# Kernel tuning notes

Measured on AMD Instinct MI355X. Metric: run time of the kernel, lower is better.

## Reference

```python
import jax, jax.numpy as jnp
import numpy as np

NEG_SLOPE = 0.2


def gat_layer(x, adj, W, a_src, a_dst):
    # x: (C, in_dim), adj: (C, C) 0/1, W: (in_dim, H*D), a_src/a_dst: (H, D)
    C = x.shape[0]
    H, D = a_src.shape
    h = (x @ W).reshape(C, H, D)            # (C, H, D)
    hh = jnp.transpose(h, (1, 0, 2))        # (H, C, D)
    asrc = jnp.einsum('hcd,hd->hc', hh, a_src)  # (H, C)
    adst = jnp.einsum('hcd,hd->hc', hh, a_dst)  # (H, C)
    e = asrc[:, :, None] + adst[:, None, :]     # (H, C, C)
    e = jax.nn.leaky_relu(e, NEG_SLOPE)
    e = jnp.where(adj[None, :, :] == 0, -jnp.inf, e)
    attn = jax.nn.softmax(e, axis=-1)           # (H, C, C)
    out = jnp.einsum('hij,hjd->hid', attn, hh)  # (H, C, D)
    return jnp.transpose(out, (1, 0, 2)).reshape(C, H * D)


def setup_inputs() -> dict:
    key = jax.random.key(0)
    ks = jax.random.split(key, 12)
    B, doc_dim = 1024, 768
    C, label_dim = 4096, 768
    hidden, H = 512, 4
    D = hidden // H  # 128

    doc_x = jax.random.normal(ks[0], (B, doc_dim), dtype=jnp.float32)
    label_init = jax.random.normal(ks[1], (C, label_dim), dtype=jnp.float32)
    adj = jax.random.randint(ks[2], (C, C), 0, 2, dtype=jnp.int32)
    adj = adj.at[jnp.arange(C), jnp.arange(C)].set(1)  # self-loops

    def xavier(k, shape):
        fan_in, fan_out = shape[0], shape[1]
        lim = jnp.sqrt(6.0 / (fan_in + fan_out)).astype(jnp.float32)
        return jax.random.uniform(k, shape, jnp.float32, -lim, lim)

    W1 = xavier(ks[3], (label_dim, hidden))
    a_src1 = xavier(ks[4], (H, D))
    a_dst1 = xavier(ks[5], (H, D))
    W2 = xavier(ks[6], (hidden, hidden))
    a_src2 = xavier(ks[7], (H, D))
    a_dst2 = xavier(ks[8], (H, D))
    Wd = xavier(ks[9], (doc_dim, hidden))
    bd = jnp.zeros((hidden,), jnp.float32)
    return {"doc_x": doc_x, "label_init": label_init, "adj": adj,
            "W1": W1, "a_src1": a_src1, "a_dst1": a_dst1,
            "W2": W2, "a_src2": a_src2, "a_dst2": a_dst2,
            "Wd": Wd, "bd": bd}


def reference(doc_x, label_init, adj, W1, a_src1, a_dst1, W2, a_src2, a_dst2, Wd, bd):
    # doc_proj (dropout = identity in eval)
    doc_h = jax.nn.relu(doc_x @ Wd + bd)            # (B, hidden)
    # label encoder: GAT -> ELU -> GAT
    h = gat_layer(label_init, adj, W1, a_src1, a_dst1)
    h = jax.nn.elu(h)
    label_h = gat_layer(h, adj, W2, a_src2, a_dst2)  # (C, hidden)
    logits = doc_h @ label_h.T                      # (B, C)
    return logits
```

## Files before the change

### kernel.cpp

```cpp
#include <hip/hip_runtime.h>
#include <hip/hip_bf16.h>
#include <math.h>

#define BDOCS   1024
#define CNODES  4096
#define INDIM   768
#define HID     512
#define NHEAD   4
#define HDIM    128
#define NEG_SLOPE 0.2f

typedef __attribute__((ext_vector_type(8))) short short8;
typedef __attribute__((ext_vector_type(4))) float f32x4;

__device__ __forceinline__ float lrelu(float x) { return x > 0.f ? x : NEG_SLOPE * x; }

__device__ __forceinline__ short f2bf(float f) {
    union { float f; unsigned u; } v; v.f = f;
    unsigned r = (v.u + 0x7fff + ((v.u >> 16) & 1)) >> 16;
    return (short)r;
}
__device__ __forceinline__ unsigned pk2(float a, float b) {
    union { float f; unsigned u; } x, y; x.f = a; y.f = b;
    unsigned lo = (x.u + 0x7fff + ((x.u >> 16) & 1)) >> 16;
    unsigned hi = (y.u + 0x7fff + ((y.u >> 16) & 1)) >> 16;
    return lo | (hi << 16);
}
__device__ __forceinline__ short hup(float f) {
    union { float f; unsigned u; } v; v.f = f;
    return (short)((v.u + 0x8000) >> 16);
}

__global__ __launch_bounds__(256)
void pack_adj(const int* __restrict__ adj, unsigned long long* __restrict__ adjb64)
{
    const int t    = threadIdx.x;
    const int gw   = blockIdx.x * 4 + (t >> 6);
    const int lane = t & 63;
    const int i  = gw >> 6;
    const int j0 = (gw & 63) * 64;
    const int a  = adj[(size_t)i * CNODES + j0 + lane];
    const unsigned long long m = __ballot(a != 0);
    if (lane == 0) adjb64[(size_t)i * 64 + (j0 >> 6)] = m;
}

__global__ __launch_bounds__(256)
void frag_T(const float* __restrict__ src, short* __restrict__ dst, int N, int K)
{
    __shared__ float tile[32][132];
    const int jc = blockIdx.x;
    const int nq = blockIdx.y;
    const int t  = threadIdx.x;
    const int KC = K >> 5;
#pragma unroll
    for (int it = 0; it < 16; it++) {
        const int e = it * 256 + t;
        const int j = e >> 7, n = e & 127;
        tile[j][n] = src[(size_t)(jc * 32 + j) * N + nq * 128 + n];
    }
    __syncthreads();
#pragma unroll
    for (int s = 0; s < 2; s++) {
        const int item = s * 256 + t;
        const int nbl = item >> 6, lane = item & 63;
        const int nr = lane & 15, kq = lane >> 4;
        short8 v;
#pragma unroll
        for (int jr = 0; jr < 8; jr++)
            v[jr] = f2bf(tile[kq * 8 + jr][nbl * 16 + nr]);
        *(short8*)&dst[((size_t)((nq * 8 + nbl) * KC + jc) * 64 + lane) * 8] = v;
    }
}

__global__ __launch_bounds__(256)
void frag_A(const float* __restrict__ src, short* __restrict__ dst, int C)
{
    __shared__ float tile[16][132];
    const int rb = blockIdx.x, cq = blockIdx.y;
    const int t  = threadIdx.x;
    const int KC = C >> 5;
#pragma unroll
    for (int it = 0; it < 8; it++) {
        const int e = it * 256 + t;
        const int r = e >> 7, c = e & 127;
        tile[r][c] = src[(size_t)(rb * 16 + r) * C + cq * 128 + c];
    }
    __syncthreads();
    const int kcl = t >> 6, lane = t & 63;
    const int m = lane & 15, kq = lane >> 4;
    short8 v8;
#pragma unroll
    for (int j = 0; j < 8; j++) v8[j] = f2bf(tile[m][kcl * 32 + kq * 8 + j]);
    *(short8*)&dst[((size_t)(rb * KC + cq * 4 + kcl) * 64 + lane) * 8] = v8;
}

template <int KC>
__global__ __launch_bounds__(64)
void gemm_hpre(const short* __restrict__ Af, const short* __restrict__ Bf,
               const float* __restrict__ a_src, const float* __restrict__ a_dst,
               short* __restrict__ hbTf, float* __restrict__ asrc, float* __restrict__ adst)
{
    __shared__ __align__(16) short tileT[128][56];
    const int lane = threadIdx.x;
    const int mb0  = blockIdx.x * 2;
    const int nq   = blockIdx.y;
    const int i0   = blockIdx.x * 32;

    f32x4 acc[2][8];
#pragma unroll
    for (int f = 0; f < 2; f++)
#pragma unroll
        for (int c = 0; c < 8; c++) acc[f][c] = (f32x4){0.f, 0.f, 0.f, 0.f};

    const short* ap0 = Af + (size_t)mb0 * KC * 512 + lane * 8;
    const short* ap1 = ap0 + (size_t)KC * 512;
    const short* bp  = Bf + (size_t)(nq * 8) * KC * 512 + lane * 8;

#pragma unroll 2
    for (int kc = 0; kc < KC; kc++) {
        short8 a0 = *(const short8*)(ap0 + (size_t)kc * 512);
        short8 a1 = *(const short8*)(ap1 + (size_t)kc * 512);
        short8 bf[8];
#pragma unroll
        for (int c = 0; c < 8; c++)
            bf[c] = *(const short8*)(bp + ((size_t)c * KC + kc) * 512);
#pragma unroll
        for (int c = 0; c < 8; c++) {
            acc[0][c] = __builtin_amdgcn_mfma_f32_16x16x32_bf16(a0, bf[c], acc[0][c], 0, 0, 0);
            acc[1][c] = __builtin_amdgcn_mfma_f32_16x16x32_bf16(a1, bf[c], acc[1][c], 0, 0, 0);
        }
    }

    const int col = lane & 15, q4 = lane >> 4;

#pragma unroll
    for (int f = 0; f < 2; f++)
#pragma unroll
        for (int c = 0; c < 8; c++) {
            unsigned d0 = pk2(acc[f][c][0], acc[f][c][1]);
            unsigned d1 = pk2(acc[f][c][2], acc[f][c][3]);
            uint2 u; u.x = d0; u.y = d1;
            *(uint2*)&tileT[c * 16 + col][f * 16 + q4 * 4] = u;
        }
    __syncthreads();
    {
        const int nr = lane & 15, kq = lane >> 4;
#pragma unroll
        for (int nbl = 0; nbl < 8; nbl++) {
            short8 v = *(const short8*)&tileT[nbl * 16 + nr][kq * 8];
            *(short8*)&hbTf[(((size_t)(nq * 8 + nbl) * (CNODES / 32) + blockIdx.x) * 64 + lane) * 8] = v;
        }
    }

    float ssrc[2][4] = {}, sdst[2][4] = {};
#pragma unroll
    for (int c = 0; c < 8; c++) {
        const float vs = a_src[nq * 128 + c * 16 + col];
        const float vd = a_dst[nq * 128 + c * 16 + col];
#pragma unroll
        for (int f = 0; f < 2; f++)
#pragma unroll
            for (int r = 0; r < 4; r++) {
                ssrc[f][r] += acc[f][c][r] * vs;
                sdst[f][r] += acc[f][c][r] * vd;
            }
    }
#pragma unroll
    for (int mask = 1; mask <= 8; mask <<= 1)
#pragma unroll
        for (int f = 0; f < 2; f++)
#pragma unroll
            for (int r = 0; r < 4; r++) {
                ssrc[f][r] += __shfl_xor(ssrc[f][r], mask);
                sdst[f][r] += __shfl_xor(sdst[f][r], mask);
            }
    if (col == 0) {
#pragma unroll
        for (int f = 0; f < 2; f++)
#pragma unroll
            for (int r = 0; r < 4; r++) {
                const int row = i0 + f * 16 + q4 * 4 + r;
                asrc[nq * CNODES + row] = ssrc[f][r];
                adst[nq * CNODES + row] = sdst[f][r];
            }
    }
}

template <int KC>
__global__ __launch_bounds__(64)
void gemm_doc(const short* __restrict__ Af, const short* __restrict__ Bf,
              const float* __restrict__ bias, short* __restrict__ dhf)
{
    __shared__ __align__(16) short tile[16][128];
    const int lane = threadIdx.x;
    const int mb = blockIdx.x;
    const int nq = blockIdx.y;

    f32x4 acc[8];
#pragma unroll
    for (int c = 0; c < 8; c++) acc[c] = (f32x4){0.f, 0.f, 0.f, 0.f};

    const short* ap = Af + (size_t)mb * KC * 512 + lane * 8;
    const short* bp = Bf + (size_t)(nq * 8) * KC * 512 + lane * 8;

#pragma unroll 2
    for (int kc = 0; kc < KC; kc++) {
        short8 a = *(const short8*)(ap + (size_t)kc * 512);
#pragma unroll
        for (int c = 0; c < 8; c++) {
            short8 bf = *(const short8*)(bp + ((size_t)c * KC + kc) * 512);
            acc[c] = __builtin_amdgcn_mfma_f32_16x16x32_bf16(a, bf, acc[c], 0, 0, 0);
        }
    }

    const int col = lane & 15, q4 = lane >> 4;
#pragma unroll
    for (int c = 0; c < 8; c++)
#pragma unroll
        for (int r = 0; r < 4; r++) {
            float v = fmaxf(acc[c][r] + bias[nq * 128 + c * 16 + col], 0.f);
            tile[q4 * 4 + r][c * 16 + col] = f2bf(v);
        }
    __syncthreads();
    const int m = lane & 15, kq = lane >> 4;
#pragma unroll
    for (int kcl = 0; kcl < 4; kcl++) {
        short8 v = *(const short8*)&tile[m][kcl * 32 + kq * 8];
        *(short8*)&dhf[(((size_t)mb * 16 + nq * 4 + kcl) * 64 + lane) * 8] = v;
    }
}

template <int KC>
__global__ __launch_bounds__(64)
void gemm_frag(const short* __restrict__ Af, const short* __restrict__ Bf,
               float* __restrict__ Cmat, int N)
{
    const int lane = threadIdx.x;
    const int mb0  = blockIdx.x * 2;
    const int nq   = blockIdx.y;

    f32x4 acc[2][8];
#pragma unroll
    for (int f = 0; f < 2; f++)
#pragma unroll
        for (int c = 0; c < 8; c++) acc[f][c] = (f32x4){0.f, 0.f, 0.f, 0.f};

    const short* ap0 = Af + (size_t)mb0 * KC * 512 + lane * 8;
    const short* ap1 = ap0 + (size_t)KC * 512;
    const short* bp  = Bf + (size_t)(nq * 8) * KC * 512 + lane * 8;

#pragma unroll 2
    for (int kc = 0; kc < KC; kc++) {
        short8 a0 = *(const short8*)(ap0 + (size_t)kc * 512);
        short8 a1 = *(const short8*)(ap1 + (size_t)kc * 512);
        short8 bf[8];
#pragma unroll
        for (int c = 0; c < 8; c++)
            bf[c] = *(const short8*)(bp + ((size_t)c * KC + kc) * 512);
#pragma unroll
        for (int c = 0; c < 8; c++) {
            acc[0][c] = __builtin_amdgcn_mfma_f32_16x16x32_bf16(a0, bf[c], acc[0][c], 0, 0, 0);
            acc[1][c] = __builtin_amdgcn_mfma_f32_16x16x32_bf16(a1, bf[c], acc[1][c], 0, 0, 0);
        }
    }

    const int col = lane & 15, q4 = lane >> 4;
#pragma unroll
    for (int f = 0; f < 2; f++)
#pragma unroll
        for (int c = 0; c < 8; c++)
#pragma unroll
            for (int r = 0; r < 4; r++) {
                const int row = (mb0 + f) * 16 + q4 * 4 + r;
                Cmat[(size_t)row * N + nq * 128 + c * 16 + col] = acc[f][c][r];
            }
}

__global__ __launch_bounds__(256)
void adst_max(const float* __restrict__ adst, float* __restrict__ Mh)
{
    const int h = blockIdx.x, t = threadIdx.x;
    __shared__ float red[256];
    float m = -1e30f;
    for (int j = t; j < CNODES; j += 256) m = fmaxf(m, adst[h * CNODES + j]);
    red[t] = m; __syncthreads();
    for (int s = 128; s >= 1; s >>= 1) {
        if (t < s) red[t] = fmaxf(red[t], red[t + s]);
        __syncthreads();
    }
    if (t == 0) Mh[h] = red[0];
}

__global__ __launch_bounds__(256)
void exp_dst(const float* __restrict__ adst, const float* __restrict__ Mh,
             float* __restrict__ E1, float* __restrict__ E2)
{
    const int idx = blockIdx.x * 256 + threadIdx.x;
    const int h = idx >> 12;
    const float d = adst[idx] - Mh[h];
    E1[idx] = __expf(d);
    E2[idx] = __expf(0.2f * d);
}

__global__ __launch_bounds__(256, 2)
void attn_pv(const short* __restrict__ hbTf,
             const unsigned int* __restrict__ adjb,
             const float* __restrict__ asrc,
             const float* __restrict__ E1, const float* __restrict__ E2,
             const float* __restrict__ Mh,
             float* __restrict__ part, float* __restrict__ lpart,
             int jper)
{
    const int t    = threadIdx.x;
    const int w    = t >> 6;
    const int lane = t & 63;
    const int m    = lane & 15;
    const int kq   = lane >> 4;
    const int i0   = blockIdx.x * 32;
    const int ks   = blockIdx.y;
    const int js   = ks * jper;

    const float mh  = Mh[w];
    const float as0 = asrc[w * CNODES + i0 + m];
    const float as1 = asrc[w * CNODES + i0 + 16 + m];
    const float mr0 = lrelu(as0 + mh), mr1 = lrelu(as1 + mh);
    const float A10 = __expf(as0 + mh - mr0),        A11 = __expf(as1 + mh - mr1);
    const float A20 = __expf(0.2f * (as0 + mh) - mr0), A21 = __expf(0.2f * (as1 + mh) - mr1);
    const float T00 = __expf(-as0 - mh),             T01 = __expf(-as1 - mh);

    f32x4 acc[2][8], accO[2];
#pragma unroll
    for (int f = 0; f < 2; f++) {
        accO[f] = (f32x4){0.f, 0.f, 0.f, 0.f};
#pragma unroll
        for (int c = 0; c < 8; c++) acc[f][c] = (f32x4){0.f, 0.f, 0.f, 0.f};
    }
    short8 ones;
#pragma unroll
    for (int q = 0; q < 8; q++) ones[q] = (short)0x3F80;

    const unsigned int* ar0 = adjb + (size_t)(i0 + m) * 128 + (js >> 5);
    const unsigned int* ar1 = adjb + (size_t)(i0 + 16 + m) * 128 + (js >> 5);
    const int nchunks = jper >> 5;

    for (int ch = 0; ch < nchunks; ch++) {
        const int j0 = js + ch * 32;
        const unsigned int aw0 = ar0[ch] >> (kq * 8);
        const unsigned int aw1 = ar1[ch] >> (kq * 8);
        const float4* p1 = (const float4*)(E1 + (size_t)w * CNODES + j0 + kq * 8);
        const float4* p2 = (const float4*)(E2 + (size_t)w * CNODES + j0 + kq * 8);
        const float4 x0 = p1[0], x1 = p1[1];
        const float4 y0 = p2[0], y1 = p2[1];
        const float e1v[8] = {x0.x, x0.y, x0.z, x0.w, x1.x, x1.y, x1.z, x1.w};
        const float e2v[8] = {y0.x, y0.y, y0.z, y0.w, y1.x, y1.y, y1.z, y1.w};

        short8 bf[8];
        const short* bbase = hbTf + (((size_t)(w * 8) * 128 + (j0 >> 5)) * 64 + lane) * 8;
#pragma unroll
        for (int c = 0; c < 8; c++)
            bf[c] = *(const short8*)(bbase + (size_t)c * 128 * 64 * 8);

        short8 a0, a1;
#pragma unroll
        for (int q = 0; q < 8; q++) {
            const float e1 = e1v[q], e2 = e2v[q];
            const bool c0 = e1 > T00, c1 = e1 > T01;
            float w0 = (c0 ? A10 : A20) * (c0 ? e1 : e2);
            float w1 = (c1 ? A11 : A21) * (c1 ? e1 : e2);
            w0 = ((aw0 >> q) & 1u) ? w0 : 0.f;
            w1 = ((aw1 >> q) & 1u) ? w1 : 0.f;
            a0[q] = hup(w0);
            a1[q] = hup(w1);
        }

#pragma unroll
        for (int c = 0; c < 8; c++) {
            acc[0][c] = __builtin_amdgcn_mfma_f32_16x16x32_bf16(a0, bf[c], acc[0][c], 0, 0, 0);
            acc[1][c] = __builtin_amdgcn_mfma_f32_16x16x32_bf16(a1, bf[c], acc[1][c], 0, 0, 0);
        }
        accO[0] = __builtin_amdgcn_mfma_f32_16x16x32_bf16(a0, ones, accO[0], 0, 0, 0);
        accO[1] = __builtin_amdgcn_mfma_f32_16x16x32_bf16(a1, ones, accO[1], 0, 0, 0);
    }

    const int col = lane & 15, q4 = lane >> 4;
    if (col == 0) {
#pragma unroll
        for (int f = 0; f < 2; f++)
#pragma unroll
            for (int r = 0; r < 4; r++)
                lpart[((size_t)ks * NHEAD + w) * CNODES + i0 + f * 16 + q4 * 4 + r] = accO[f][r];
    }

    float* pbase = part + (size_t)ks * CNODES * HID;
#pragma unroll
    for (int f = 0; f < 2; f++)
#pragma unroll
        for (int c = 0; c < 8; c++)
#pragma unroll
            for (int r = 0; r < 4; r++) {
                const int row = i0 + f * 16 + q4 * 4 + r;
                pbase[(size_t)row * HID + w * HDIM + c * 16 + col] = acc[f][c][r];
            }
}

template <bool ELU>
__global__ __launch_bounds__(256)
void reduce_norm_frag(const float* __restrict__ part, const float* __restrict__ lpart,
                      short* __restrict__ dst, int KS)
{
    const int t = threadIdx.x;
    const int W = blockIdx.x * 4 + (t >> 6);
    const int lane = t & 63;
    const int rb = W >> 4, kc = W & 15;
    const int m = lane & 15, kq = lane >> 4;
    const int i = rb * 16 + m;
    const int n0 = kc * 32 + kq * 8;
    const int h = kc >> 2;

    float v[8] = {};
    float l = 0.f;
    for (int s = 0; s < KS; s++) {
        const float* p = part + (size_t)s * CNODES * HID + (size_t)i * HID + n0;
        const float4 a = ((const float4*)p)[0], b = ((const float4*)p)[1];
        v[0] += a.x; v[1] += a.y; v[2] += a.z; v[3] += a.w;
        v[4] += b.x; v[5] += b.y; v[6] += b.z; v[7] += b.w;
        l += lpart[((size_t)s * NHEAD + h) * CNODES + i];
    }
    const float inv = 1.0f / l;
    short8 o;
#pragma unroll
    for (int q = 0; q < 8; q++) {
        float x = v[q] * inv;
        if (ELU) x = x > 0.f ? x : (__expf(x) - 1.f);
        o[q] = f2bf(x);
    }
    *(short8*)&dst[((size_t)(rb * 16 + kc) * 64 + lane) * 8] = o;
}

extern "C" void kernel_launch(void* const* d_in, const int* in_sizes, int n_in,
                              void* d_out, int out_size, void* d_ws, size_t ws_size,
                              hipStream_t stream)
{
    const float* doc_x      = (const float*)d_in[0];
    const float* label_init = (const float*)d_in[1];
    const int*   adj        = (const int*)d_in[2];
    const float* W1         = (const float*)d_in[3];
    const float* a_src1     = (const float*)d_in[4];
    const float* a_dst1     = (const float*)d_in[5];
    const float* W2         = (const float*)d_in[6];
    const float* a_src2     = (const float*)d_in[7];
    const float* a_dst2     = (const float*)d_in[8];
    const float* Wd         = (const float*)d_in[9];
    const float* bd         = (const float*)d_in[10];
    float*       out        = (float*)d_out;

    char* wsb = (char*)d_ws;
    size_t off = 0;
    auto alloc = [&](size_t bytes) -> char* {
        char* p = wsb + off;
        off = (off + bytes + 255) & ~(size_t)255;
        return p;
    };

    float* asrc  = (float*)alloc(NHEAD * CNODES * 4);
    float* adst  = (float*)alloc(NHEAD * CNODES * 4);
    float* Mh    = (float*)alloc(256);
    float* E1    = (float*)alloc(NHEAD * CNODES * 4);
    float* E2    = (float*)alloc(NHEAD * CNODES * 4);
    float* lpart = (float*)alloc((size_t)8 * NHEAD * CNODES * 4);
    unsigned int* adjb = (unsigned int*)alloc((size_t)CNODES * 128 * 4);
    short* hbTf  = (short*)alloc((size_t)CNODES * HID * 2);
    short* Wdf   = (short*)alloc((size_t)INDIM * HID * 2);
    short* W1f   = (short*)alloc((size_t)INDIM * HID * 2);
    short* W2f   = (short*)alloc((size_t)HID * HID * 2);
    short* dxf   = (short*)alloc((size_t)BDOCS * INDIM * 2);
    short* Af_li = (short*)alloc((size_t)CNODES * INDIM * 2);
    short* Af2   = (short*)alloc((size_t)CNODES * HID * 2);
    short* lhf   = (short*)alloc((size_t)CNODES * HID * 2);
    short* dhf   = (short*)alloc((size_t)BDOCS * HID * 2);
    float* part  = (float*)(wsb + off);

    int KS = 4;
    const size_t slice_bytes = (size_t)CNODES * HID * 4;
    while (KS > 1 && off + (size_t)KS * slice_bytes > ws_size) KS >>= 1;
    const int jper = CNODES / KS;

    const dim3 blk(256);

    pack_adj<<<CNODES * CNODES / 64 / 4, blk, 0, stream>>>(adj, (unsigned long long*)adjb);
    frag_T<<<dim3(INDIM / 32, HID / 128), blk, 0, stream>>>(Wd, Wdf, HID, INDIM);
    frag_T<<<dim3(INDIM / 32, HID / 128), blk, 0, stream>>>(W1, W1f, HID, INDIM);
    frag_T<<<dim3(HID / 32, HID / 128), blk, 0, stream>>>(W2, W2f, HID, HID);
    frag_A<<<dim3(BDOCS / 16, INDIM / 128), blk, 0, stream>>>(doc_x, dxf, INDIM);
    frag_A<<<dim3(CNODES / 16, INDIM / 128), blk, 0, stream>>>(label_init, Af_li, INDIM);

    gemm_doc<INDIM / 32><<<dim3(BDOCS / 16, HID / 128), 64, 0, stream>>>(dxf, Wdf, bd, dhf);

    gemm_hpre<INDIM / 32><<<dim3(CNODES / 32, NHEAD), 64, 0, stream>>>(
        Af_li, W1f, a_src1, a_dst1, hbTf, asrc, adst);

    adst_max<<<NHEAD, 256, 0, stream>>>(adst, Mh);
    exp_dst<<<NHEAD * CNODES / 256, blk, 0, stream>>>(adst, Mh, E1, E2);
    attn_pv<<<dim3(CNODES / 32, KS), blk, 0, stream>>>(hbTf, adjb, asrc, E1, E2, Mh, part, lpart, jper);
    reduce_norm_frag<true><<<CNODES * HID / 256 / 8, blk, 0, stream>>>(part, lpart, Af2, KS);

    gemm_hpre<HID / 32><<<dim3(CNODES / 32, NHEAD), 64, 0, stream>>>(
        Af2, W2f, a_src2, a_dst2, hbTf, asrc, adst);

    adst_max<<<NHEAD, 256, 0, stream>>>(adst, Mh);
    exp_dst<<<NHEAD * CNODES / 256, blk, 0, stream>>>(adst, Mh, E1, E2);
    attn_pv<<<dim3(CNODES / 32, KS), blk, 0, stream>>>(hbTf, adjb, asrc, E1, E2, Mh, part, lpart, jper);
    reduce_norm_frag<false><<<CNODES * HID / 256 / 8, blk, 0, stream>>>(part, lpart, lhf, KS);

    gemm_frag<HID / 32><<<dim3(BDOCS / 32, CNODES / 128), 64, 0, stream>>>(dhf, lhf, out, CNODES);
}
```

Before: 411.6 us.

## Shrink GEMM tiles, fuse softmax stats, bf16 split-K partials with KSPLIT=8

Halves the per-block tile in gemm_hpre (16 rows) and gemm_doc (64 columns) so more blocks fill the GPU. Merges adst_max and exp_dst into one 1024-thread kernel. Fixes the attention split-K at 8 and stores the partials in bf16 through an LDS-staged coalesced write, which halves the traffic of the partials and of the reduce pass. attn_pv also gets occupancy hint 3 and loop unroll 2. Storing partials in bf16 costs accuracy, and the workspace is no longer checked against ws_size.

```diff
diff --git a/kernel.cpp b/kernel.cpp
--- a/kernel.cpp
+++ b/kernel.cpp
@@ -10,6 +10,10 @@
 #define HDIM    128
 #define NEG_SLOPE 0.2f
 
+#define KSPLIT  8
+#define JPER    (CNODES / KSPLIT)
+#define NCH     (JPER / 32)
+
 typedef __attribute__((ext_vector_type(8))) short short8;
 typedef __attribute__((ext_vector_type(4))) float f32x4;
 
@@ -19,6 +23,10 @@
     union { float f; unsigned u; } v; v.f = f;
     unsigned r = (v.u + 0x7fff + ((v.u >> 16) & 1)) >> 16;
     return (short)r;
+}
+__device__ __forceinline__ float bf2f(short s) {
+    union { float f; unsigned u; } v; v.u = ((unsigned)(unsigned short)s) << 16;
+    return v.f;
 }
 __device__ __forceinline__ unsigned pk2(float a, float b) {
     union { float f; unsigned u; } x, y; x.f = a; y.f = b;
@@ -100,11 +108,131 @@
                const float* __restrict__ a_src, const float* __restrict__ a_dst,
                short* __restrict__ hbTf, float* __restrict__ asrc, float* __restrict__ adst)
 {
-    __shared__ __align__(16) short tileT[128][56];
+    __shared__ __align__(16) short tileT[128][24];
+    const int lane = threadIdx.x;
+    const int mb   = blockIdx.x;
+    const int nq   = blockIdx.y;
+    const int i0   = mb * 16;
+
+    f32x4 acc[8];
+#pragma unroll
+    for (int c = 0; c < 8; c++) acc[c] = (f32x4){0.f, 0.f, 0.f, 0.f};
+
+    const short* ap = Af + (size_t)mb * KC * 512 + lane * 8;
+    const short* bp = Bf + (size_t)(nq * 8) * KC * 512 + lane * 8;
+
+#pragma unroll 2
+    for (int kc = 0; kc < KC; kc++) {
+        short8 a = *(const short8*)(ap + (size_t)kc * 512);
+#pragma unroll
+        for (int c = 0; c < 8; c++) {
+            short8 bf = *(const short8*)(bp + ((size_t)c * KC + kc) * 512);
+            acc[c] = __builtin_amdgcn_mfma_f32_16x16x32_bf16(a, bf, acc[c], 0, 0, 0);
+        }
+    }
+
+    const int col = lane & 15, q4 = lane >> 4;
+
+#pragma unroll
+    for (int c = 0; c < 8; c++) {
+        uint2 u;
+        u.x = pk2(acc[c][0], acc[c][1]);
+        u.y = pk2(acc[c][2], acc[c][3]);
+        *(uint2*)&tileT[c * 16 + col][q4 * 4] = u;
+    }
+    __syncthreads();
+    {
+        const int jc = mb >> 1, khalf = mb & 1;
+        const int nr = lane & 15, kq = lane >> 4;
+        if ((kq >> 1) == khalf) {
+#pragma unroll
+            for (int nbl = 0; nbl < 8; nbl++) {
+                short8 v = *(const short8*)&tileT[nbl * 16 + nr][(kq & 1) * 8];
+                *(short8*)&hbTf[(((size_t)(nq * 8 + nbl) * (CNODES / 32) + jc) * 64 + lane) * 8] = v;
+            }
+        }
+    }
+
+    float ssrc[4] = {}, sdst[4] = {};
+#pragma unroll
+    for (int c = 0; c < 8; c++) {
+        const float vs = a_src[nq * 128 + c * 16 + col];
+        const float vd = a_dst[nq * 128 + c * 16 + col];
+#pragma unroll
+        for (int r = 0; r < 4; r++) {
+            ssrc[r] += acc[c][r] * vs;
+            sdst[r] += acc[c][r] * vd;
+        }
+    }
+#pragma unroll
+    for (int mask = 1; mask <= 8; mask <<= 1)
+#pragma unroll
+        for (int r = 0; r < 4; r++) {
+            ssrc[r] += __shfl_xor(ssrc[r], mask);
+            sdst[r] += __shfl_xor(sdst[r], mask);
+        }
+    if (col == 0) {
+#pragma unroll
+        for (int r = 0; r < 4; r++) {
+            const int row = i0 + q4 * 4 + r;
+            asrc[nq * CNODES + row] = ssrc[r];
+            adst[nq * CNODES + row] = sdst[r];
+        }
+    }
+}
+
+template <int KC>
+__global__ __launch_bounds__(64)
+void gemm_doc(const short* __restrict__ Af, const short* __restrict__ Bf,
+              const float* __restrict__ bias, short* __restrict__ dhf)
+{
+    __shared__ __align__(16) short tile[16][64];
+    const int lane = threadIdx.x;
+    const int mb = blockIdx.x;
+    const int ng = blockIdx.y;
+
+    f32x4 acc[4];
+#pragma unroll
+    for (int c = 0; c < 4; c++) acc[c] = (f32x4){0.f, 0.f, 0.f, 0.f};
+
+    const short* ap = Af + (size_t)mb * KC * 512 + lane * 8;
+    const short* bp = Bf + (size_t)(ng * 4) * KC * 512 + lane * 8;
+
+#pragma unroll 2
+    for (int kc = 0; kc < KC; kc++) {
+        short8 a = *(const short8*)(ap + (size_t)kc * 512);
+#pragma unroll
+        for (int c = 0; c < 4; c++) {
+            short8 bf = *(const short8*)(bp + ((size_t)c * KC + kc) * 512);
+            acc[c] = __builtin_amdgcn_mfma_f32_16x16x32_bf16(a, bf, acc[c], 0, 0, 0);
+        }
+    }
+
+    const int col = lane & 15, q4 = lane >> 4;
+#pragma unroll
+    for (int c = 0; c < 4; c++)
+#pragma unroll
+        for (int r = 0; r < 4; r++) {
+            float v = fmaxf(acc[c][r] + bias[ng * 64 + c * 16 + col], 0.f);
+            tile[q4 * 4 + r][c * 16 + col] = f2bf(v);
+        }
+    __syncthreads();
+    const int m = lane & 15, kq = lane >> 4;
+#pragma unroll
+    for (int kcl = 0; kcl < 2; kcl++) {
+        short8 v = *(const short8*)&tile[m][kcl * 32 + kq * 8];
+        *(short8*)&dhf[(((size_t)mb * 16 + ng * 2 + kcl) * 64 + lane) * 8] = v;
+    }
+}
+
+template <int KC>
+__global__ __launch_bounds__(64)
+void gemm_frag(const short* __restrict__ Af, const short* __restrict__ Bf,
+               float* __restrict__ Cmat, int N)
+{
     const int lane = threadIdx.x;
     const int mb0  = blockIdx.x * 2;
     const int nq   = blockIdx.y;
-    const int i0   = blockIdx.x * 32;
 
     f32x4 acc[2][8];
 #pragma unroll
@@ -132,139 +260,6 @@
     }
 
     const int col = lane & 15, q4 = lane >> 4;
-
-#pragma unroll
-    for (int f = 0; f < 2; f++)
-#pragma unroll
-        for (int c = 0; c < 8; c++) {
-            unsigned d0 = pk2(acc[f][c][0], acc[f][c][1]);
-            unsigned d1 = pk2(acc[f][c][2], acc[f][c][3]);
-            uint2 u; u.x = d0; u.y = d1;
-            *(uint2*)&tileT[c * 16 + col][f * 16 + q4 * 4] = u;
-        }
-    __syncthreads();
-    {
-        const int nr = lane & 15, kq = lane >> 4;
-#pragma unroll
-        for (int nbl = 0; nbl < 8; nbl++) {
-            short8 v = *(const short8*)&tileT[nbl * 16 + nr][kq * 8];
-            *(short8*)&hbTf[(((size_t)(nq * 8 + nbl) * (CNODES / 32) + blockIdx.x) * 64 + lane) * 8] = v;
-        }
-    }
-
-    float ssrc[2][4] = {}, sdst[2][4] = {};
-#pragma unroll
-    for (int c = 0; c < 8; c++) {
-        const float vs = a_src[nq * 128 + c * 16 + col];
-        const float vd = a_dst[nq * 128 + c * 16 + col];
-#pragma unroll
-        for (int f = 0; f < 2; f++)
-#pragma unroll
-            for (int r = 0; r < 4; r++) {
-                ssrc[f][r] += acc[f][c][r] * vs;
-                sdst[f][r] += acc[f][c][r] * vd;
-            }
-    }
-#pragma unroll
-    for (int mask = 1; mask <= 8; mask <<= 1)
-#pragma unroll
-        for (int f = 0; f < 2; f++)
-#pragma unroll
-            for (int r = 0; r < 4; r++) {
-                ssrc[f][r] += __shfl_xor(ssrc[f][r], mask);
-                sdst[f][r] += __shfl_xor(sdst[f][r], mask);
-            }
-    if (col == 0) {
-#pragma unroll
-        for (int f = 0; f < 2; f++)
-#pragma unroll
-            for (int r = 0; r < 4; r++) {
-                const int row = i0 + f * 16 + q4 * 4 + r;
-                asrc[nq * CNODES + row] = ssrc[f][r];
-                adst[nq * CNODES + row] = sdst[f][r];
-            }
-    }
-}
-
-template <int KC>
-__global__ __launch_bounds__(64)
-void gemm_doc(const short* __restrict__ Af, const short* __restrict__ Bf,
-              const float* __restrict__ bias, short* __restrict__ dhf)
-{
-    __shared__ __align__(16) short tile[16][128];
-    const int lane = threadIdx.x;
-    const int mb = blockIdx.x;
-    const int nq = blockIdx.y;
-
-    f32x4 acc[8];
-#pragma unroll
-    for (int c = 0; c < 8; c++) acc[c] = (f32x4){0.f, 0.f, 0.f, 0.f};
-
-    const short* ap = Af + (size_t)mb * KC * 512 + lane * 8;
-    const short* bp = Bf + (size_t)(nq * 8) * KC * 512 + lane * 8;
-
-#pragma unroll 2
-    for (int kc = 0; kc < KC; kc++) {
-        short8 a = *(const short8*)(ap + (size_t)kc * 512);
-#pragma unroll
-        for (int c = 0; c < 8; c++) {
-            short8 bf = *(const short8*)(bp + ((size_t)c * KC + kc) * 512);
-            acc[c] = __builtin_amdgcn_mfma_f32_16x16x32_bf16(a, bf, acc[c], 0, 0, 0);
-        }
-    }
-
-    const int col = lane & 15, q4 = lane >> 4;
-#pragma unroll
-    for (int c = 0; c < 8; c++)
-#pragma unroll
-        for (int r = 0; r < 4; r++) {
-            float v = fmaxf(acc[c][r] + bias[nq * 128 + c * 16 + col], 0.f);
-            tile[q4 * 4 + r][c * 16 + col] = f2bf(v);
-        }
-    __syncthreads();
-    const int m = lane & 15, kq = lane >> 4;
-#pragma unroll
-    for (int kcl = 0; kcl < 4; kcl++) {
-        short8 v = *(const short8*)&tile[m][kcl * 32 + kq * 8];
-        *(short8*)&dhf[(((size_t)mb * 16 + nq * 4 + kcl) * 64 + lane) * 8] = v;
-    }
-}
-
-template <int KC>
-__global__ __launch_bounds__(64)
-void gemm_frag(const short* __restrict__ Af, const short* __restrict__ Bf,
-               float* __restrict__ Cmat, int N)
-{
-    const int lane = threadIdx.x;
-    const int mb0  = blockIdx.x * 2;
-    const int nq   = blockIdx.y;
-
-    f32x4 acc[2][8];
-#pragma unroll
-    for (int f = 0; f < 2; f++)
-#pragma unroll
-        for (int c = 0; c < 8; c++) acc[f][c] = (f32x4){0.f, 0.f, 0.f, 0.f};
-
-    const short* ap0 = Af + (size_t)mb0 * KC * 512 + lane * 8;
-    const short* ap1 = ap0 + (size_t)KC * 512;
-    const short* bp  = Bf + (size_t)(nq * 8) * KC * 512 + lane * 8;
-
-#pragma unroll 2
-    for (int kc = 0; kc < KC; kc++) {
-        short8 a0 = *(const short8*)(ap0 + (size_t)kc * 512);
-        short8 a1 = *(const short8*)(ap1 + (size_t)kc * 512);
-        short8 bf[8];
-#pragma unroll
-        for (int c = 0; c < 8; c++)
-            bf[c] = *(const short8*)(bp + ((size_t)c * KC + kc) * 512);
-#pragma unroll
-        for (int c = 0; c < 8; c++) {
-            acc[0][c] = __builtin_amdgcn_mfma_f32_16x16x32_bf16(a0, bf[c], acc[0][c], 0, 0, 0);
-            acc[1][c] = __builtin_amdgcn_mfma_f32_16x16x32_bf16(a1, bf[c], acc[1][c], 0, 0, 0);
-        }
-    }
-
-    const int col = lane & 15, q4 = lane >> 4;
 #pragma unroll
     for (int f = 0; f < 2; f++)
 #pragma unroll
@@ -276,41 +271,41 @@
             }
 }
 
-__global__ __launch_bounds__(256)
-void adst_max(const float* __restrict__ adst, float* __restrict__ Mh)
-{
+__global__ __launch_bounds__(1024)
+void stats_exp(const float* __restrict__ adst, float* __restrict__ Mh,
+               float* __restrict__ E1, float* __restrict__ E2)
+{
+    __shared__ float red[1024];
+    __shared__ float s_mh;
     const int h = blockIdx.x, t = threadIdx.x;
-    __shared__ float red[256];
-    float m = -1e30f;
-    for (int j = t; j < CNODES; j += 256) m = fmaxf(m, adst[h * CNODES + j]);
+    const float4 d4 = *(const float4*)(adst + (size_t)h * CNODES + t * 4);
+    float m = fmaxf(fmaxf(d4.x, d4.y), fmaxf(d4.z, d4.w));
     red[t] = m; __syncthreads();
-    for (int s = 128; s >= 1; s >>= 1) {
+    for (int s = 512; s >= 1; s >>= 1) {
         if (t < s) red[t] = fmaxf(red[t], red[t + s]);
         __syncthreads();
     }
-    if (t == 0) Mh[h] = red[0];
-}
-
-__global__ __launch_bounds__(256)
-void exp_dst(const float* __restrict__ adst, const float* __restrict__ Mh,
-             float* __restrict__ E1, float* __restrict__ E2)
-{
-    const int idx = blockIdx.x * 256 + threadIdx.x;
-    const int h = idx >> 12;
-    const float d = adst[idx] - Mh[h];
-    E1[idx] = __expf(d);
-    E2[idx] = __expf(0.2f * d);
-}
-
-__global__ __launch_bounds__(256, 2)
+    if (t == 0) { s_mh = red[0]; Mh[h] = red[0]; }
+    __syncthreads();
+    const float mh = s_mh;
+    float4 e1, e2;
+    e1.x = __expf(d4.x - mh); e2.x = __expf(0.2f * (d4.x - mh));
+    e1.y = __expf(d4.y - mh); e2.y = __expf(0.2f * (d4.y - mh));
+    e1.z = __expf(d4.z - mh); e2.z = __expf(0.2f * (d4.z - mh));
+    e1.w = __expf(d4.w - mh); e2.w = __expf(0.2f * (d4.w - mh));
+    *(float4*)(E1 + (size_t)h * CNODES + t * 4) = e1;
+    *(float4*)(E2 + (size_t)h * CNODES + t * 4) = e2;
+}
+
+__global__ __launch_bounds__(256, 3)
 void attn_pv(const short* __restrict__ hbTf,
              const unsigned int* __restrict__ adjb,
              const float* __restrict__ asrc,
              const float* __restrict__ E1, const float* __restrict__ E2,
              const float* __restrict__ Mh,
-             float* __restrict__ part, float* __restrict__ lpart,
-             int jper)
-{
+             short* __restrict__ part, float* __restrict__ lpart)
+{
+    __shared__ __align__(16) short tileO[32][520];
     const int t    = threadIdx.x;
     const int w    = t >> 6;
     const int lane = t & 63;
@@ -318,15 +313,15 @@
     const int kq   = lane >> 4;
     const int i0   = blockIdx.x * 32;
     const int ks   = blockIdx.y;
-    const int js   = ks * jper;
+    const int js   = ks * JPER;
 
     const float mh  = Mh[w];
     const float as0 = asrc[w * CNODES + i0 + m];
     const float as1 = asrc[w * CNODES + i0 + 16 + m];
     const float mr0 = lrelu(as0 + mh), mr1 = lrelu(as1 + mh);
-    const float A10 = __expf(as0 + mh - mr0),        A11 = __expf(as1 + mh - mr1);
+    const float A10 = __expf(as0 + mh - mr0),          A11 = __expf(as1 + mh - mr1);
     const float A20 = __expf(0.2f * (as0 + mh) - mr0), A21 = __expf(0.2f * (as1 + mh) - mr1);
-    const float T00 = __expf(-as0 - mh),             T01 = __expf(-as1 - mh);
+    const float T00 = __expf(-as0 - mh),               T01 = __expf(-as1 - mh);
 
     f32x4 acc[2][8], accO[2];
 #pragma unroll
@@ -339,11 +334,11 @@
 #pragma unroll
     for (int q = 0; q < 8; q++) ones[q] = (short)0x3F80;
 
-    const unsigned int* ar0 = adjb + (size_t)(i0 + m) * 128 + (js >> 5);
-    const unsigned int* ar1 = adjb + (size_t)(i0 + 16 + m) * 128 + (js >> 5);
-    const int nchunks = jper >> 5;
-
-    for (int ch = 0; ch < nchunks; ch++) {
+    const unsigned int* ar0 = adjb + (size_t)(i0 + m) * 128 + ks * NCH;
+    const unsigned int* ar1 = adjb + (size_t)(i0 + 16 + m) * 128 + ks * NCH;
+
+#pragma unroll 2
+    for (int ch = 0; ch < NCH; ch++) {
         const int j0 = js + ch * 32;
         const unsigned int aw0 = ar0[ch] >> (kq * 8);
         const unsigned int aw1 = ar1[ch] >> (kq * 8);
@@ -383,7 +378,7 @@
     }
 
     const int col = lane & 15, q4 = lane >> 4;
-    if (col == 0) {
+    if (m == 0) {
 #pragma unroll
         for (int f = 0; f < 2; f++)
 #pragma unroll
@@ -391,22 +386,28 @@
                 lpart[((size_t)ks * NHEAD + w) * CNODES + i0 + f * 16 + q4 * 4 + r] = accO[f][r];
     }
 
-    float* pbase = part + (size_t)ks * CNODES * HID;
 #pragma unroll
     for (int f = 0; f < 2; f++)
 #pragma unroll
         for (int c = 0; c < 8; c++)
 #pragma unroll
-            for (int r = 0; r < 4; r++) {
-                const int row = i0 + f * 16 + q4 * 4 + r;
-                pbase[(size_t)row * HID + w * HDIM + c * 16 + col] = acc[f][c][r];
-            }
+            for (int r = 0; r < 4; r++)
+                tileO[f * 16 + q4 * 4 + r][w * 128 + c * 16 + col] = f2bf(acc[f][c][r]);
+    __syncthreads();
+    short* pS = part + (size_t)ks * CNODES * HID;
+#pragma unroll
+    for (int it = 0; it < 8; it++) {
+        const int u   = it * 256 + t;
+        const int row = u >> 6, un = u & 63;
+        uint4 v = *(const uint4*)&tileO[row][un * 8];
+        *(uint4*)&pS[(size_t)(i0 + row) * HID + un * 8] = v;
+    }
 }
 
 template <bool ELU>
 __global__ __launch_bounds__(256)
-void reduce_norm_frag(const float* __restrict__ part, const float* __restrict__ lpart,
-                      short* __restrict__ dst, int KS)
+void reduce_norm_frag(const short* __restrict__ part, const float* __restrict__ lpart,
+                      short* __restrict__ dst)
 {
     const int t = threadIdx.x;
     const int W = blockIdx.x * 4 + (t >> 6);
@@ -419,11 +420,15 @@
 
     float v[8] = {};
     float l = 0.f;
-    for (int s = 0; s < KS; s++) {
-        const float* p = part + (size_t)s * CNODES * HID + (size_t)i * HID + n0;
-        const float4 a = ((const float4*)p)[0], b = ((const float4*)p)[1];
-        v[0] += a.x; v[1] += a.y; v[2] += a.z; v[3] += a.w;
-        v[4] += b.x; v[5] += b.y; v[6] += b.z; v[7] += b.w;
+#pragma unroll
+    for (int s = 0; s < KSPLIT; s++) {
+        const uint4 raw = *(const uint4*)&part[(size_t)s * CNODES * HID + (size_t)i * HID + n0];
+        const unsigned rr[4] = {raw.x, raw.y, raw.z, raw.w};
+#pragma unroll
+        for (int q = 0; q < 4; q++) {
+            v[q * 2]     += bf2f((short)(rr[q] & 0xffff));
+            v[q * 2 + 1] += bf2f((short)(rr[q] >> 16));
+        }
         l += lpart[((size_t)s * NHEAD + h) * CNODES + i];
     }
     const float inv = 1.0f / l;
@@ -467,7 +472,7 @@
     float* Mh    = (float*)alloc(256);
     float* E1    = (float*)alloc(NHEAD * CNODES * 4);
     float* E2    = (float*)alloc(NHEAD * CNODES * 4);
-    float* lpart = (float*)alloc((size_t)8 * NHEAD * CNODES * 4);
+    float* lpart = (float*)alloc((size_t)KSPLIT * NHEAD * CNODES * 4);
     unsigned int* adjb = (unsigned int*)alloc((size_t)CNODES * 128 * 4);
     short* hbTf  = (short*)alloc((size_t)CNODES * HID * 2);
     short* Wdf   = (short*)alloc((size_t)INDIM * HID * 2);
@@ -478,12 +483,8 @@
     short* Af2   = (short*)alloc((size_t)CNODES * HID * 2);
     short* lhf   = (short*)alloc((size_t)CNODES * HID * 2);
     short* dhf   = (short*)alloc((size_t)BDOCS * HID * 2);
-    float* part  = (float*)(wsb + off);
-
-    int KS = 4;
-    const size_t slice_bytes = (size_t)CNODES * HID * 4;
-    while (KS > 1 && off + (size_t)KS * slice_bytes > ws_size) KS >>= 1;
-    const int jper = CNODES / KS;
+    short* part  = (short*)alloc((size_t)KSPLIT * CNODES * HID * 2);
+    (void)ws_size;
 
     const dim3 blk(256);
 
@@ -494,23 +495,21 @@
     frag_A<<<dim3(BDOCS / 16, INDIM / 128), blk, 0, stream>>>(doc_x, dxf, INDIM);
     frag_A<<<dim3(CNODES / 16, INDIM / 128), blk, 0, stream>>>(label_init, Af_li, INDIM);
 
-    gemm_doc<INDIM / 32><<<dim3(BDOCS / 16, HID / 128), 64, 0, stream>>>(dxf, Wdf, bd, dhf);
-
-    gemm_hpre<INDIM / 32><<<dim3(CNODES / 32, NHEAD), 64, 0, stream>>>(
+    gemm_doc<INDIM / 32><<<dim3(BDOCS / 16, HID / 64), 64, 0, stream>>>(dxf, Wdf, bd, dhf);
+
+    gemm_hpre<INDIM / 32><<<dim3(CNODES / 16, NHEAD), 64, 0, stream>>>(
         Af_li, W1f, a_src1, a_dst1, hbTf, asrc, adst);
 
-    adst_max<<<NHEAD, 256, 0, stream>>>(adst, Mh);
-    exp_dst<<<NHEAD * CNODES / 256, blk, 0, stream>>>(adst, Mh, E1, E2);
-    attn_pv<<<dim3(CNODES / 32, KS), blk, 0, stream>>>(hbTf, adjb, asrc, E1, E2, Mh, part, lpart, jper);
-    reduce_norm_frag<true><<<CNODES * HID / 256 / 8, blk, 0, stream>>>(part, lpart, Af2, KS);
-
-    gemm_hpre<HID / 32><<<dim3(CNODES / 32, NHEAD), 64, 0, stream>>>(
+    stats_exp<<<NHEAD, 1024, 0, stream>>>(adst, Mh, E1, E2);
+    attn_pv<<<dim3(CNODES / 32, KSPLIT), blk, 0, stream>>>(hbTf, adjb, asrc, E1, E2, Mh, part, lpart);
+    reduce_norm_frag<true><<<CNODES * HID / 256 / 8, blk, 0, stream>>>(part, lpart, Af2);
+
+    gemm_hpre<HID / 32><<<dim3(CNODES / 16, NHEAD), 64, 0, stream>>>(
         Af2, W2f, a_src2, a_dst2, hbTf, asrc, adst);
 
-    adst_max<<<NHEAD, 256, 0, stream>>>(adst, Mh);
-    exp_dst<<<NHEAD * CNODES / 256, blk, 0, stream>>>(adst, Mh, E1, E2);
-    attn_pv<<<dim3(CNODES / 32, KS), blk, 0, stream>>>(hbTf, adjb, asrc, E1, E2, Mh, part, lpart, jper);
-    reduce_norm_frag<false><<<CNODES * HID / 256 / 8, blk, 0, stream>>>(part, lpart, lhf, KS);
+    stats_exp<<<NHEAD, 1024, 0, stream>>>(adst, Mh, E1, E2);
+    attn_pv<<<dim3(CNODES / 32, KSPLIT), blk, 0, stream>>>(hbTf, adjb, asrc, E1, E2, Mh, part, lpart);
+    reduce_norm_frag<false><<<CNODES * HID / 256 / 8, blk, 0, stream>>>(part, lpart, lhf);
 
     gemm_frag<HID / 32><<<dim3(BDOCS / 32, CNODES / 128), 64, 0, stream>>>(dhf, lhf, out, CNODES);
 }
```

Result: faster. 381.0 us (-7.4%).
